# Kernel tuning notes

Measured on AMD Instinct MI355X. Metric: run time of the kernel, lower is better.

## Reference

```python
import jax, jax.numpy as jnp
import numpy as np

B, D, H, C = 8192, 1024, 128, 16


def setup_inputs() -> dict:
    key = jax.random.key(0)
    ks = jax.random.split(key, 6)
    x = jax.random.normal(ks[0], (B, D), dtype=jnp.float32)
    c = jax.random.randint(ks[1], (B,), 0, C, dtype=jnp.int32)
    # per-condition 2-layer MLP params (fc1: D->H, fc2: H->D), torch Linear layout [out,in]
    W1 = jax.random.normal(ks[2], (C, H, D), dtype=jnp.float32) * 0.02
    b1 = jax.random.normal(ks[3], (C, H), dtype=jnp.float32) * 0.02
    W2 = jax.random.normal(ks[4], (C, D, H), dtype=jnp.float32) * 0.02
    b2 = jax.random.normal(ks[5], (C, D), dtype=jnp.float32) * 0.02
    return {"x": x, "c": c, "W1": W1, "b1": b1, "W2": W2, "b2": b2}


def reference(x, c, W1, b1, W2, b2):
    # embeddingnet treated as identity: embedded_x = x  [B, D]
    # Hard condition routing: compute every condition's mini-MLP densely, then
    # select the row matching each sample's condition (jit-friendly grouped GEMM).
    h_all = jnp.einsum('bd,chd->cbh', x, W1) + b1[:, None, :]          # [C, B, H]
    out_all = jnp.einsum('cbh,cdh->cbd', h_all, W2) + b2[:, None, :]   # [C, B, D]
    masked = out_all[c, jnp.arange(x.shape[0])]                        # [B, D]
    # l2_embed = True branch
    norm = jnp.linalg.norm(masked, axis=1, keepdims=True) + 1e-10
    masked = masked / norm
    mask_norm = jnp.float32(0.0)
    embed_norm = jnp.linalg.norm(x)
    return (masked, mask_norm, embed_norm, x)
```

## Files before the change

### kernel.cpp

```cpp
#include <hip/hip_runtime.h>
#include <hip/hip_bf16.h>
#include <math.h>

#define B_ 8192
#define D_ 1024
#define H_ 128
#define C_ 16
#define BD (B_*D_)
#define SUBR 16
#define SLOTS 68
#define MAXSUB 150
#define GRID_F (8 * SLOTS)

using bf16x8 = __attribute__((ext_vector_type(8))) __bf16;
using f32x4  = __attribute__((ext_vector_type(4))) float;
typedef unsigned short ushort_t;


__device__ inline bf16x8 cvt8(float4 a, float4 b) {
    bf16x8 r;
    r[0] = (__bf16)a.x; r[1] = (__bf16)a.y; r[2] = (__bf16)a.z; r[3] = (__bf16)a.w;
    r[4] = (__bf16)b.x; r[5] = (__bf16)b.y; r[6] = (__bf16)b.z; r[7] = (__bf16)b.w;
    return r;
}
__device__ inline unsigned pack2(float a, float b) {
    unsigned ua = __builtin_bit_cast(unsigned short, (__bf16)a);
    unsigned ub = __builtin_bit_cast(unsigned short, (__bf16)b);
    return ua | (ub << 16);
}

__global__ __launch_bounds__(256) void k_prep(const float* __restrict__ W1f,
                                              const float* __restrict__ W2f,
                                              const int* __restrict__ c,
                                              const float* __restrict__ x,
                                              __bf16* __restrict__ w1s,
                                              __bf16* __restrict__ w2s,
                                              __bf16* __restrict__ xbf,
                                              int* __restrict__ w,
                                              float* __restrict__ xpart,
                                              float* __restrict__ out) {
    __shared__ ulong2 stg[2048];
    bf16x8* stgv = (bf16x8*)stg;
    int bid = blockIdx.x, tid = threadIdx.x;

    if (bid < 128) {
        size_t mbase = (size_t)bid * 2048;
#pragma unroll
        for (int u = 0; u < 8; ++u) {
            int ml = u * 256 + tid;
            const float* src = W1f + (mbase + ml) * 8;
            float4 f0 = *(const float4*)src, f1 = *(const float4*)(src + 4);
            int row = ml >> 7, cc8 = ml & 127;
            stgv[row * 128 + (cc8 ^ (row & 7))] = cvt8(f0, f1);
        }
        __syncthreads();
#pragma unroll
        for (int u = 0; u < 8; ++u) {
            int o = u * 256 + tid;
            int ks = o >> 6, kg = (o >> 4) & 3, l15 = o & 15;
            bf16x8 v = stgv[l15 * 128 + ((ks * 4 + kg) ^ (l15 & 7))];
            *(bf16x8*)(w1s + (mbase + o) * 8) = v;
        }
    } else if (bid < 256) {
        int b = bid - 128;
        size_t mbase = (size_t)b * 2048;
#pragma unroll
        for (int u = 0; u < 8; ++u) {
            int ml = u * 256 + tid;
            const float* src = W2f + (mbase + ml) * 8;
            float4 f0 = *(const float4*)src, f1 = *(const float4*)(src + 4);
            int rr = ml >> 4, cc8 = ml & 15;
            stgv[rr * 16 + (cc8 ^ (rr & 15))] = cvt8(f0, f1);
        }
        __syncthreads();
#pragma unroll
        for (int u = 0; u < 8; ++u) {
            int o = u * 256 + tid;
            int jfr = o >> 8, ks = (o >> 6) & 3, kg = (o >> 4) & 3, l15 = o & 15;
            int rr = jfr * 16 + l15, cc8 = ks * 4 + kg;
            bf16x8 v = stgv[rr * 16 + (cc8 ^ (rr & 15))];
            *(bf16x8*)(w2s + (mbase + o) * 8) = v;
        }
    } else if (bid == 256) {
        __shared__ int hist[C_], base[C_], poff[C_], nt[C_];
        if (tid < C_) hist[tid] = 0;
        __syncthreads();
        for (int i = tid; i < B_; i += 256) atomicAdd(&hist[c[i]], 1);
        __syncthreads();
        if (tid == 0) {
            int off = 0;
            for (int cc = 0; cc < C_; ++cc) {
                nt[cc] = (hist[cc] + SUBR - 1) >> 4;
                poff[cc] = off;
                base[cc] = off;
                off += nt[cc] * SUBR;
            }
        }
        __syncthreads();
        if (tid < C_) {
            int cc = tid, xcd = cc >> 1;
            int s0 = (cc & 1) ? nt[cc - 1] : 0;
            int end = poff[cc] + hist[cc];
            for (int t = 0; t < nt[cc]; ++t) {
                int* e = &w[32 + (xcd * MAXSUB + s0 + t) * 3];
                e[0] = cc; e[1] = poff[cc] + t * SUBR; e[2] = end;
            }
            if ((cc & 1) == 0) w[16 + xcd] = nt[cc] + nt[cc + 1];
        }
        __syncthreads();
        for (int i = tid; i < B_; i += 256) {
            int pos = atomicAdd(&base[c[i]], 1);
            w[8192 + pos] = i;
        }
    } else {
        int xb = bid - 257;
        size_t base0 = (size_t)xb * 8192;
        float xsq = 0.0f;
#pragma unroll
        for (int u = 0; u < 8; ++u) {
            size_t idx = base0 + u * 1024 + tid * 4;
            float4 f = *(const float4*)(x + idx);
            *(uint2*)(xbf + idx) = make_uint2(pack2(f.x, f.y), pack2(f.z, f.w));
            float2* xo = (float2*)(out + (size_t)BD + 2 + idx);
            xo[0] = make_float2(f.x, f.y);
            xo[1] = make_float2(f.z, f.w);
            xsq += f.x*f.x + f.y*f.y + f.z*f.z + f.w*f.w;
        }
        float s = xsq;
        s += __shfl_xor(s, 1);  s += __shfl_xor(s, 2);  s += __shfl_xor(s, 4);
        s += __shfl_xor(s, 8);  s += __shfl_xor(s, 16); s += __shfl_xor(s, 32);
        __shared__ float red[4];
        int lane = tid & 63, wv = tid >> 6;
        if (lane == 0) red[wv] = s;
        __syncthreads();
        if (tid == 0) xpart[xb] = red[0] + red[1] + red[2] + red[3];
    }
}

__global__ __launch_bounds__(512, 4) void k_f(const __bf16* __restrict__ xbf,
                                              const __bf16* __restrict__ w1s,
                                              const __bf16* __restrict__ w2s,
                                              const float* __restrict__ b1f,
                                              const float* __restrict__ b2f,
                                              const int* __restrict__ wsi,
                                              const float* __restrict__ xpart,
                                              float* __restrict__ out) {
    int xcd = blockIdx.x & 7, slot0 = blockIdx.x >> 3;
    int nsub = wsi[16 + xcd];
    const int* sidx = wsi + 8192;

    __shared__ ulong2 xot_raw[2048];
    __shared__ ushort_t Hs[16 * 128];
    __shared__ float sqs[16 * 8];
    char* ldsx = (char*)xot_raw;
    unsigned* Ot32 = (unsigned*)xot_raw;

    int tid = threadIdx.x, wv = tid >> 6, lane = tid & 63, l15 = lane & 15, kg = lane >> 4;
    int sr = wv * 2 + (lane >> 5);
    int cg = lane & 31;
    int skg = cg & 3, skb = cg >> 2;

    if (blockIdx.x == GRID_F - 1) {
        float v = xpart[tid] + xpart[tid + 512];
        v += __shfl_xor(v, 1);  v += __shfl_xor(v, 2);  v += __shfl_xor(v, 4);
        v += __shfl_xor(v, 8);  v += __shfl_xor(v, 16); v += __shfl_xor(v, 32);
        if (lane == 0) sqs[wv] = v;
        __syncthreads();
        if (tid == 0) {
            float e = sqs[0] + sqs[1] + sqs[2] + sqs[3] + sqs[4] + sqs[5] + sqs[6] + sqs[7];
            out[BD] = 0.0f;
            out[BD + 1] = sqrtf(e);
        }
        __syncthreads();
    }

    for (int si = slot0; si < nsub; si += SLOTS) {
        const int* e = wsi + 32 + (xcd * MAXSUB + si) * 3;
        int cond = e[0], prow0 = e[1], end = e[2];

        {
            int pr = prow0 + sr;
            int orow = sidx[pr < end ? pr : (end - 1)];
            const char* xs = (const char*)xbf + (size_t)orow * 2048;
#pragma unroll
            for (int it = 0; it < 4; ++it) {
                int m = it * 32 + cg;
                bf16x8 v = *(const bf16x8*)(xs + m * 16);
                int ks = it * 8 + skb;
                *(bf16x8*)(ldsx + ks * 1024 + skg * 256 + ((sr ^ skb) * 16)) = v;
            }
        }
        __syncthreads();

        const char* bA = (const char*)w1s + (size_t)cond * 262144 + wv * 32768 + lane * 16;
        f32x4 acc = {};
#pragma unroll 1
        for (int kb = 0; kb < 4; ++kb) {
            bf16x8 b0 = *(const bf16x8*)(bA + (kb * 8 + 0) * 1024);
            bf16x8 b1 = *(const bf16x8*)(bA + (kb * 8 + 1) * 1024);
            bf16x8 b2 = *(const bf16x8*)(bA + (kb * 8 + 2) * 1024);
            bf16x8 b3 = *(const bf16x8*)(bA + (kb * 8 + 3) * 1024);
            bf16x8 b4 = *(const bf16x8*)(bA + (kb * 8 + 4) * 1024);
            bf16x8 b5 = *(const bf16x8*)(bA + (kb * 8 + 5) * 1024);
            bf16x8 b6 = *(const bf16x8*)(bA + (kb * 8 + 6) * 1024);
            bf16x8 b7 = *(const bf16x8*)(bA + (kb * 8 + 7) * 1024);
#pragma unroll
            for (int j = 0; j < 8; ++j) {
                int ks = kb * 8 + j;
                bf16x8 x0 = *(const bf16x8*)(ldsx + ks * 1024 + kg * 256 + ((l15 ^ (ks & 7)) * 16));
                bf16x8 bj = j == 0 ? b0 : j == 1 ? b1 : j == 2 ? b2 : j == 3 ? b3
                          : j == 4 ? b4 : j == 5 ? b5 : j == 6 ? b6 : b7;
                acc = __builtin_amdgcn_mfma_f32_16x16x32_bf16(x0, bj, acc, 0, 0, 0);
            }
        }
        __syncthreads();

        {
            int j0 = wv * 16 + l15;
            float bias = b1f[cond * 128 + j0];
            int sl0 = j0 >> 3, jb = j0 & 7;
#pragma unroll
            for (int v = 0; v < 4; ++v) {
                int r0 = kg * 4 + v;
                __bf16 h0 = (__bf16)(acc[v] + bias);
                Hs[r0 * 128 + ((sl0 ^ (r0 & 7)) * 8) + jb] = __builtin_bit_cast(ushort_t, h0);
            }
        }
        __syncthreads();

        bf16x8 pa[4];
#pragma unroll
        for (int i = 0; i < 4; ++i)
            pa[i] = *(const bf16x8*)(Hs + l15 * 128 + (((i * 4 + kg) ^ (l15 & 7)) * 8));

        const char* w2b = (const char*)w2s + (size_t)cond * 262144 + wv * 32768 + lane * 16;
        float sq[4] = {0.f, 0.f, 0.f, 0.f};
        unsigned cswz = (unsigned)((kg & 1) << 4);
#pragma unroll 1
        for (int f = 0; f < 8; ++f) {
            const char* wb = w2b + f * 4096;
            bf16x8 q0 = *(const bf16x8*)(wb);
            bf16x8 q1 = *(const bf16x8*)(wb + 1024);
            bf16x8 q2 = *(const bf16x8*)(wb + 2048);
            bf16x8 q3 = *(const bf16x8*)(wb + 3072);
            f32x4 c0 = {};
            c0 = __builtin_amdgcn_mfma_f32_16x16x32_bf16(pa[0], q0, c0, 0, 0, 0);
            c0 = __builtin_amdgcn_mfma_f32_16x16x32_bf16(pa[1], q1, c0, 0, 0, 0);
            c0 = __builtin_amdgcn_mfma_f32_16x16x32_bf16(pa[2], q2, c0, 0, 0, 0);
            c0 = __builtin_amdgcn_mfma_f32_16x16x32_bf16(pa[3], q3, c0, 0, 0, 0);
            int jg = (wv * 8 + f) * 16 + l15;
            float bias = b2f[cond * 1024 + jg];
            float t0 = c0[0] + bias, t1 = c0[1] + bias, t2 = c0[2] + bias, t3 = c0[3] + bias;
            sq[0] += t0*t0; sq[1] += t1*t1; sq[2] += t2*t2; sq[3] += t3*t3;
            unsigned jc = (unsigned)jg ^ cswz;
            Ot32[(kg * 2    ) * 1024 + jc] = pack2(t0, t1);
            Ot32[(kg * 2 + 1) * 1024 + jc] = pack2(t2, t3);
        }
#pragma unroll
        for (int v = 0; v < 4; ++v) {
            float s = sq[v];
            s += __shfl_xor(s, 1); s += __shfl_xor(s, 2);
            s += __shfl_xor(s, 4); s += __shfl_xor(s, 8);
            if (l15 == 0) sqs[(kg * 4 + v) * 8 + wv] = s;
        }
        __syncthreads();

#pragma unroll 1
        for (int rr = 0; rr < 2; ++rr) {
            int r = wv * 2 + rr;
            int pr = prow0 + r;
            if (pr < end) {
                int orow = sidx[pr];
                float s = sqs[r*8+0] + sqs[r*8+1] + sqs[r*8+2] + sqs[r*8+3]
                        + sqs[r*8+4] + sqs[r*8+5] + sqs[r*8+6] + sqs[r*8+7];
                float inv = 1.0f / (sqrtf(s) + 1e-10f);
                int hi = (r & 1) * 16;
                unsigned rswz = (unsigned)(((r >> 2) & 1) << 4);
                const unsigned* base = Ot32 + (r >> 1) * 1024;
                float4* go = (float4*)(out + (size_t)orow * D_);
#pragma unroll
                for (int it = 0; it < 4; ++it) {
                    unsigned cu = (unsigned)(lane * 4 + it * 256) ^ rswz;
                    uint4 u = *(const uint4*)(base + cu);
                    float4 v;
                    v.x = (float)__builtin_bit_cast(__bf16, (ushort_t)(u.x >> hi)) * inv;
                    v.y = (float)__builtin_bit_cast(__bf16, (ushort_t)(u.y >> hi)) * inv;
                    v.z = (float)__builtin_bit_cast(__bf16, (ushort_t)(u.z >> hi)) * inv;
                    v.w = (float)__builtin_bit_cast(__bf16, (ushort_t)(u.w >> hi)) * inv;
                    go[lane + it * 64] = v;
                }
            }
        }
        __syncthreads();
    }
}

extern "C" void kernel_launch(void* const* d_in, const int* in_sizes, int n_in,
                              void* d_out, int out_size, void* d_ws, size_t ws_size,
                              hipStream_t stream) {
    const float* x  = (const float*)d_in[0];
    const int*   c  = (const int*)d_in[1];
    const float* W1 = (const float*)d_in[2];
    const float* b1 = (const float*)d_in[3];
    const float* W2 = (const float*)d_in[4];
    const float* b2 = (const float*)d_in[5];
    float* out = (float*)d_out;
    char* ws = (char*)d_ws;
    int* wsi = (int*)ws;
    float* xpart = (float*)(ws + 131072);
    __bf16* w1s  = (__bf16*)(ws + 262144);
    __bf16* w2s  = (__bf16*)(ws + 4456448);
    __bf16* xbf  = (__bf16*)(ws + 8650752);

    k_prep<<<1281, 256, 0, stream>>>(W1, W2, c, x, w1s, w2s, xbf, wsi, xpart, out);
    k_f<<<GRID_F, 512, 0, stream>>>(xbf, w1s, w2s, b1, b2, wsi, xpart, out);
}
```

Before: 64.76 us.

## Drop bf16 x staging; read fp32 x directly and move copy/norm into main kernel

The prep kernel no longer converts x to a bf16 workspace copy. The MLP blocks now read fp32 rows of x and convert to bf16 while staging into LDS. The x passthrough copy and the squared-norm reduction move into extra blocks of the main kernel, finished by a last-block atomic counter. This removes a 16MB bf16 write and read and lets the copy overlap the GEMM work, at the cost of doubling x read bytes in the gather and adding an atomic/threadfence reduction.

```diff
diff --git a/kernel.cpp b/kernel.cpp
--- a/kernel.cpp
+++ b/kernel.cpp
@@ -10,7 +10,9 @@
 #define SUBR 16
 #define SLOTS 68
 #define MAXSUB 150
-#define GRID_F (8 * SLOTS)
+#define GRID_MLP 544
+#define GRID_COPY 512
+#define GRID_F (GRID_MLP + GRID_COPY)
 
 using bf16x8 = __attribute__((ext_vector_type(8))) __bf16;
 using f32x4  = __attribute__((ext_vector_type(4))) float;
@@ -32,13 +34,9 @@
 __global__ __launch_bounds__(256) void k_prep(const float* __restrict__ W1f,
                                               const float* __restrict__ W2f,
                                               const int* __restrict__ c,
-                                              const float* __restrict__ x,
                                               __bf16* __restrict__ w1s,
                                               __bf16* __restrict__ w2s,
-                                              __bf16* __restrict__ xbf,
-                                              int* __restrict__ w,
-                                              float* __restrict__ xpart,
-                                              float* __restrict__ out) {
+                                              int* __restrict__ w) {
     __shared__ ulong2 stg[2048];
     bf16x8* stgv = (bf16x8*)stg;
     int bid = blockIdx.x, tid = threadIdx.x;
@@ -81,9 +79,10 @@
             bf16x8 v = stgv[rr * 16 + (cc8 ^ (rr & 15))];
             *(bf16x8*)(w2s + (mbase + o) * 8) = v;
         }
-    } else if (bid == 256) {
+    } else {
         __shared__ int hist[C_], base[C_], poff[C_], nt[C_];
         if (tid < C_) hist[tid] = 0;
+        if (tid == 0) w[24] = 0;
         __syncthreads();
         for (int i = tid; i < B_; i += 256) atomicAdd(&hist[c[i]], 1);
         __syncthreads();
@@ -112,15 +111,34 @@
             int pos = atomicAdd(&base[c[i]], 1);
             w[8192 + pos] = i;
         }
-    } else {
-        int xb = bid - 257;
-        size_t base0 = (size_t)xb * 8192;
+    }
+}
+
+__global__ __launch_bounds__(512, 4) void k_f(const float* __restrict__ x,
+                                              const __bf16* __restrict__ w1s,
+                                              const __bf16* __restrict__ w2s,
+                                              const float* __restrict__ b1f,
+                                              const float* __restrict__ b2f,
+                                              int* __restrict__ wsi,
+                                              float* __restrict__ xpart,
+                                              float* __restrict__ out) {
+    __shared__ ulong2 xot_raw[2048];
+    __shared__ ushort_t Hs[16 * 128];
+    __shared__ float sqs[16 * 8];
+    __shared__ int lastFlag;
+    char* ldsx = (char*)xot_raw;
+    unsigned* Ot32 = (unsigned*)xot_raw;
+
+    int tid = threadIdx.x, wv = tid >> 6, lane = tid & 63, l15 = lane & 15, kg = lane >> 4;
+
+    if (blockIdx.x >= GRID_MLP) {
+        int cb = blockIdx.x - GRID_MLP;
+        size_t base0 = (size_t)cb * 16384;
         float xsq = 0.0f;
 #pragma unroll
         for (int u = 0; u < 8; ++u) {
-            size_t idx = base0 + u * 1024 + tid * 4;
+            size_t idx = base0 + u * 2048 + tid * 4;
             float4 f = *(const float4*)(x + idx);
-            *(uint2*)(xbf + idx) = make_uint2(pack2(f.x, f.y), pack2(f.z, f.w));
             float2* xo = (float2*)(out + (size_t)BD + 2 + idx);
             xo[0] = make_float2(f.x, f.y);
             xo[1] = make_float2(f.z, f.w);
@@ -129,51 +147,39 @@
         float s = xsq;
         s += __shfl_xor(s, 1);  s += __shfl_xor(s, 2);  s += __shfl_xor(s, 4);
         s += __shfl_xor(s, 8);  s += __shfl_xor(s, 16); s += __shfl_xor(s, 32);
-        __shared__ float red[4];
-        int lane = tid & 63, wv = tid >> 6;
-        if (lane == 0) red[wv] = s;
-        __syncthreads();
-        if (tid == 0) xpart[xb] = red[0] + red[1] + red[2] + red[3];
+        if (lane == 0) sqs[wv] = s;
+        __syncthreads();
+        if (tid == 0) {
+            xpart[cb] = sqs[0] + sqs[1] + sqs[2] + sqs[3] + sqs[4] + sqs[5] + sqs[6] + sqs[7];
+            __threadfence();
+            int prev = atomicAdd(&wsi[24], 1);
+            lastFlag = (prev == GRID_COPY - 1);
+        }
+        __syncthreads();
+        if (lastFlag) {
+            __threadfence();
+            float v = xpart[tid];
+            v += __shfl_xor(v, 1);  v += __shfl_xor(v, 2);  v += __shfl_xor(v, 4);
+            v += __shfl_xor(v, 8);  v += __shfl_xor(v, 16); v += __shfl_xor(v, 32);
+            if (lane == 0) sqs[wv] = v;
+            __syncthreads();
+            if (tid == 0) {
+                float e = sqs[0] + sqs[1] + sqs[2] + sqs[3] + sqs[4] + sqs[5] + sqs[6] + sqs[7];
+                out[BD] = 0.0f;
+                out[BD + 1] = sqrtf(e);
+            }
+        }
+        return;
     }
-}
-
-__global__ __launch_bounds__(512, 4) void k_f(const __bf16* __restrict__ xbf,
-                                              const __bf16* __restrict__ w1s,
-                                              const __bf16* __restrict__ w2s,
-                                              const float* __restrict__ b1f,
-                                              const float* __restrict__ b2f,
-                                              const int* __restrict__ wsi,
-                                              const float* __restrict__ xpart,
-                                              float* __restrict__ out) {
+
     int xcd = blockIdx.x & 7, slot0 = blockIdx.x >> 3;
     int nsub = wsi[16 + xcd];
     const int* sidx = wsi + 8192;
 
-    __shared__ ulong2 xot_raw[2048];
-    __shared__ ushort_t Hs[16 * 128];
-    __shared__ float sqs[16 * 8];
-    char* ldsx = (char*)xot_raw;
-    unsigned* Ot32 = (unsigned*)xot_raw;
-
-    int tid = threadIdx.x, wv = tid >> 6, lane = tid & 63, l15 = lane & 15, kg = lane >> 4;
     int sr = wv * 2 + (lane >> 5);
     int cg = lane & 31;
     int skg = cg & 3, skb = cg >> 2;
 
-    if (blockIdx.x == GRID_F - 1) {
-        float v = xpart[tid] + xpart[tid + 512];
-        v += __shfl_xor(v, 1);  v += __shfl_xor(v, 2);  v += __shfl_xor(v, 4);
-        v += __shfl_xor(v, 8);  v += __shfl_xor(v, 16); v += __shfl_xor(v, 32);
-        if (lane == 0) sqs[wv] = v;
-        __syncthreads();
-        if (tid == 0) {
-            float e = sqs[0] + sqs[1] + sqs[2] + sqs[3] + sqs[4] + sqs[5] + sqs[6] + sqs[7];
-            out[BD] = 0.0f;
-            out[BD + 1] = sqrtf(e);
-        }
-        __syncthreads();
-    }
-
     for (int si = slot0; si < nsub; si += SLOTS) {
         const int* e = wsi + 32 + (xcd * MAXSUB + si) * 3;
         int cond = e[0], prow0 = e[1], end = e[2];
@@ -181,13 +187,14 @@
         {
             int pr = prow0 + sr;
             int orow = sidx[pr < end ? pr : (end - 1)];
-            const char* xs = (const char*)xbf + (size_t)orow * 2048;
+            const float* xs = x + (size_t)orow * D_;
 #pragma unroll
             for (int it = 0; it < 4; ++it) {
-                int m = it * 32 + cg;
-                bf16x8 v = *(const bf16x8*)(xs + m * 16);
+                int col0 = it * 256 + cg * 8;
+                float4 f0 = *(const float4*)(xs + col0);
+                float4 f1 = *(const float4*)(xs + col0 + 4);
                 int ks = it * 8 + skb;
-                *(bf16x8*)(ldsx + ks * 1024 + skg * 256 + ((sr ^ skb) * 16)) = v;
+                *(bf16x8*)(ldsx + ks * 1024 + skg * 256 + ((sr ^ skb) * 16)) = cvt8(f0, f1);
             }
         }
         __syncthreads();
@@ -310,8 +317,7 @@
     float* xpart = (float*)(ws + 131072);
     __bf16* w1s  = (__bf16*)(ws + 262144);
     __bf16* w2s  = (__bf16*)(ws + 4456448);
-    __bf16* xbf  = (__bf16*)(ws + 8650752);
-
-    k_prep<<<1281, 256, 0, stream>>>(W1, W2, c, x, w1s, w2s, xbf, wsi, xpart, out);
-    k_f<<<GRID_F, 512, 0, stream>>>(xbf, w1s, w2s, b1, b2, wsi, xpart, out);
-}
+
+    k_prep<<<257, 256, 0, stream>>>(W1, W2, c, w1s, w2s, wsi);
+    k_f<<<GRID_F, 512, 0, stream>>>(x, w1s, w2s, b1, b2, wsi, xpart, out);
+}
```

Result: slower. 84.35 us (+30.3%).
